# Optimization experiments

Hardware: AMD Instinct MI355X
Metric: run time of the kernel (lower is better)

The kernel has to match this reference:

```python
import jax, jax.numpy as jnp
import numpy as np

B, T, D, R = 4, 2048, 1024, 32


def setup_inputs() -> dict:
    key = jax.random.key(0)
    kx, ku = jax.random.split(key)
    x = jax.random.normal(kx, (B, T, D), dtype=jnp.float32)
    # low-rank metric factor; small init so distances are moderate
    U = jax.random.normal(ku, (D, R), dtype=jnp.float32) * 0.05
    return {"x": x, "U": U}


def reference(x, U):
    # g = U @ U.T (PSD low-rank metric).
    # dist_sq[b,t,j] = (x_t - x_j)^T g (x_t - x_j)
    #               = ||U^T x_t||^2 + ||U^T x_j||^2 - 2 (U^T x_t).(U^T x_j)
    # Algebraic expansion of the original O(B*T*T*D) broadcasted diff tensor.
    y = jnp.einsum('btd,dr->btr', x, U)                # [B,T,R]
    n = jnp.sum(y * y, axis=-1)                         # [B,T]
    cross = jnp.einsum('btr,bjr->btj', y, y)            # [B,T,T]
    dist_sq = n[:, :, None] + n[:, None, :] - 2.0 * cross
    attn = jax.nn.softmax(-dist_sq, axis=-1)            # [B,T,T]
    return jnp.einsum('btj,bjd->btd', attn, x)          # [B,T,D]
```

## Files before the change

kernel.cpp:

```cpp
#include <hip/hip_runtime.h>

#define B_ 4
#define T_ 2048
#define D_ 1024
#define R_ 32
#define XP 136

typedef __attribute__((ext_vector_type(8))) short short8;
typedef __attribute__((ext_vector_type(4))) float f32x4;
typedef __attribute__((ext_vector_type(4))) unsigned short us4;
typedef __attribute__((ext_vector_type(8))) unsigned short us8;

__device__ __forceinline__ unsigned short f2bf(float f) {
  union { float f; unsigned u; } v; v.f = f;
  unsigned r = (v.u + 0x7fffu + ((v.u >> 16) & 1u)) >> 16;
  return (unsigned short)r;
}
__device__ __forceinline__ float bf2f(unsigned short h) {
  union { unsigned u; float f; } v; v.u = (unsigned)h << 16;
  return v.f;
}

__global__ __launch_bounds__(256)
void geo_prep(const float* __restrict__ x, const float* __restrict__ U,
              unsigned short* __restrict__ xt, float* __restrict__ ypart) {
  __shared__ unsigned short xs[128 * XP];
  __shared__ unsigned short uts[32 * XP];
  const int bb = blockIdx.y, t0 = blockIdx.x * 128, d0 = blockIdx.z * 128;
  const int tid = threadIdx.x, w = tid >> 6, lane = tid & 63;
  const int m = lane & 15, quad = lane >> 4;

  f32x4 uv[4];
  #pragma unroll
  for (int p = 0; p < 4; p++) {
    const int i4 = p * 256 + tid;
    uv[p] = *(const f32x4*)(U + (size_t)(d0 + (i4 >> 3)) * R_ + (i4 & 7) * 4);
  }
  f32x4 xv[16];
  #pragma unroll
  for (int p = 0; p < 16; p++) {
    const int i4 = p * 256 + tid;
    xv[p] = *(const f32x4*)(x + ((size_t)bb * T_ + t0 + (i4 >> 5)) * D_ + d0 + (i4 & 31) * 4);
  }
  #pragma unroll
  for (int p = 0; p < 4; p++) {
    const int i4 = p * 256 + tid; const int du = i4 >> 3, ru4 = i4 & 7;
    #pragma unroll
    for (int k = 0; k < 4; k++) uts[(ru4 * 4 + k) * XP + du] = f2bf(uv[p][k]);
  }
  #pragma unroll
  for (int p = 0; p < 16; p++) {
    const int i4 = p * 256 + tid; const int r = i4 >> 5, c4 = i4 & 31;
    us4 c;
    c[0] = f2bf(xv[p][0]); c[1] = f2bf(xv[p][1]);
    c[2] = f2bf(xv[p][2]); c[3] = f2bf(xv[p][3]);
    *(us4*)&xs[r * XP + c4 * 4] = c;
  }
  __syncthreads();
  {
    const int d = tid >> 1, th = tid & 1;
    unsigned short* xo = xt + ((size_t)bb * D_ + d0 + d) * T_ + t0 + th * 64;
    #pragma unroll
    for (int i = 0; i < 8; i++) {
      us8 o;
      #pragma unroll
      for (int k = 0; k < 8; k++) o[k] = xs[(th * 64 + i * 8 + k) * XP + d];
      *(us8*)(xo + i * 8) = o;
    }
  }
  f32x4 acc[2][2];
  #pragma unroll
  for (int i = 0; i < 2; i++)
    #pragma unroll
    for (int j = 0; j < 2; j++) acc[i][j] = (f32x4){0.f, 0.f, 0.f, 0.f};
  #pragma unroll
  for (int ks = 0; ks < 4; ks++) {
    const int ko = ks * 32 + quad * 8;
    short8 a0 = *(const short8*)&xs[(w * 32 + m) * XP + ko];
    short8 a1 = *(const short8*)&xs[(w * 32 + 16 + m) * XP + ko];
    short8 b0 = *(const short8*)&uts[m * XP + ko];
    short8 b1 = *(const short8*)&uts[(16 + m) * XP + ko];
    acc[0][0] = __builtin_amdgcn_mfma_f32_16x16x32_bf16(a0, b0, acc[0][0], 0, 0, 0);
    acc[0][1] = __builtin_amdgcn_mfma_f32_16x16x32_bf16(a0, b1, acc[0][1], 0, 0, 0);
    acc[1][0] = __builtin_amdgcn_mfma_f32_16x16x32_bf16(a1, b0, acc[1][0], 0, 0, 0);
    acc[1][1] = __builtin_amdgcn_mfma_f32_16x16x32_bf16(a1, b1, acc[1][1], 0, 0, 0);
  }
  #pragma unroll
  for (int tb = 0; tb < 2; tb++)
    #pragma unroll
    for (int nb = 0; nb < 2; nb++)
      *(f32x4*)(ypart + ((size_t)(blockIdx.z * B_ + bb) * R_ + nb * 16 + m) * T_
                + t0 + w * 32 + tb * 16 + quad * 4) = acc[tb][nb];
}

__global__ __launch_bounds__(256)
void geo_reduce(const float* __restrict__ ypart, unsigned short* __restrict__ ybf,
                float* __restrict__ nsq) {
  __shared__ float ls[32][36];
  const int t0 = blockIdx.x * 32, bb = blockIdx.y;
  const int tid = threadIdx.x;
  {
    const int r = tid >> 3, t4 = (tid & 7) * 4;
    f32x4 v = {0.f, 0.f, 0.f, 0.f};
    #pragma unroll
    for (int s = 0; s < 8; s++) {
      f32x4 p = *(const f32x4*)(ypart + ((size_t)(s * B_ + bb) * R_ + r) * T_ + t0 + t4);
      #pragma unroll
      for (int k = 0; k < 4; k++) v[k] += p[k];
    }
    *(f32x4*)&ls[r][t4] = v;
  }
  __syncthreads();
  const int t = tid >> 3, r4 = (tid & 7) * 4;
  us4 pk; float part = 0.f;
  #pragma unroll
  for (int k = 0; k < 4; k++) {
    const unsigned short h = f2bf(1.69864446f * ls[r4 + k][t]);
    const float bv = bf2f(h); part += bv * bv; pk[k] = h;
  }
  *(us4*)(ybf + ((size_t)bb * T_ + t0 + t) * R_ + r4) = pk;
  part += __shfl_xor(part, 1, 64);
  part += __shfl_xor(part, 2, 64);
  part += __shfl_xor(part, 4, 64);
  if ((tid & 7) == 0) nsq[bb * T_ + t0 + t] = 0.5f * part;
}

__global__ __launch_bounds__(256, 2)
void geo_fused(const unsigned short* __restrict__ ybf,
               const float* __restrict__ nsq,
               const unsigned short* __restrict__ xt,
               float* __restrict__ out) {
  __shared__ unsigned short Bs[2][128 * 64];
  __shared__ float l_s[128];
  const int bz = blockIdx.z, id = blockIdx.x;
  const int d0 = (id & 7) * 128;
  const int t0 = (id >> 3) * 128;
  const int tid = threadIdx.x, w = tid >> 6, lane = tid & 63;
  const int m = lane & 15, quad = lane >> 4;
  const int srow = lane >> 3, sslot = lane & 7;

  const unsigned short* yb = ybf + (size_t)bz * T_ * R_;
  const float* nq = nsq + bz * T_;
  const unsigned short* Xb = xt + ((size_t)bz * D_ + d0) * T_;

#define STAGE(J0, BUF) do {                                                      \
    _Pragma("unroll")                                                            \
    for (int cc = 0; cc < 4; cc++) {                                             \
      const int rbase = w * 32 + cc * 8;                                         \
      const int row = rbase + srow;                                              \
      const int sw = (sslot ^ (row & 7)) * 8;                                    \
      __builtin_amdgcn_global_load_lds(                                          \
        (const __attribute__((address_space(1))) void*)(Xb + (size_t)row * T_ + (J0) + sw), \
        (__attribute__((address_space(3))) void*)(&Bs[BUF][rbase * 64]), 16, 0, 0); \
    } } while (0)

#define BODY(IT, AJC, NJC, AJN, NJN, BUFC, BUFN) do {                            \
    const int j0b = (IT) * 64;                                                   \
    const int jn0 = (((IT) + 1) & 31) * 64;                                      \
    _Pragma("unroll")                                                            \
    for (int ja = 0; ja < 4; ja++) {                                             \
      const int jr = 32 * (ja >> 1) + 8 * (m >> 2) + (ja & 1) * 4 + (m & 3);     \
      AJN[ja] = *(const short8*)(yb + (size_t)(jn0 + jr) * R_ + quad * 8);       \
      NJN[ja] = *(const f32x4*)(nq + jn0 + 32 * (ja >> 1) + (ja & 1) * 4 + 8 * quad); \
    }                                                                            \
    short8 pfrag[2][2];                                                          \
    _Pragma("unroll")                                                            \
    for (int tb = 0; tb < 2; tb++) {                                             \
      _Pragma("unroll")                                                          \
      for (int ja = 0; ja < 4; ja++) {                                           \
        f32x4 cin;                                                               \
        _Pragma("unroll")                                                        \
        for (int r = 0; r < 4; r++) cin[r] = nnt[tb] - NJC[ja][r];               \
        f32x4 c = __builtin_amdgcn_mfma_f32_16x16x32_bf16(AJC[ja], at[tb], cin, 0, 0, 0); \
        _Pragma("unroll")                                                        \
        for (int r = 0; r < 4; r++) {                                            \
          const float p = __builtin_amdgcn_exp2f(c[r]);                          \
          lsum4[tb][r] += p;                                                     \
          pfrag[tb][ja >> 1][(ja & 1) * 4 + r] = (short)f2bf(p);                 \
        }                                                                        \
      }                                                                          \
    }                                                                            \
    __syncthreads();                    \
    if ((IT) + 1 < 32) STAGE(j0b + 64, BUFN);                                    \
    _Pragma("unroll")                                                            \
    for (int kb = 0; kb < 2; kb++) {                                             \
      short8 bfr[8];                                                             \
      _Pragma("unroll")                                                          \
      for (int nb = 0; nb < 8; nb++)                                             \
        bfr[nb] = *(const short8*)&Bs[BUFC][(nb * 16 + m) * 64 + (((kb * 4 + quad) ^ (m & 7)) * 8)]; \
      _Pragma("unroll")                                                          \
      for (int tb = 0; tb < 2; tb++)                                             \
        _Pragma("unroll")                                                        \
        for (int nb = 0; nb < 8; nb++)                                           \
          acc[tb][nb] = __builtin_amdgcn_mfma_f32_16x16x32_bf16(pfrag[tb][kb], bfr[nb], acc[tb][nb], 0, 0, 0); \
    } } while (0)

  short8 at[2]; float nnt[2]; f32x4 lsum4[2];
  #pragma unroll
  for (int tb = 0; tb < 2; tb++) {
    at[tb] = *(const short8*)(yb + (size_t)(t0 + w * 32 + tb * 16 + m) * R_ + quad * 8);
    nnt[tb] = -nq[t0 + w * 32 + tb * 16 + m];
    lsum4[tb] = (f32x4){0.f, 0.f, 0.f, 0.f};
  }

  f32x4 acc[2][8];
  #pragma unroll
  for (int i = 0; i < 2; i++)
    #pragma unroll
    for (int j = 0; j < 8; j++) acc[i][j] = (f32x4){0.f, 0.f, 0.f, 0.f};

  short8 ajA[4], ajB[4]; f32x4 njA[4], njB[4];
  #pragma unroll
  for (int ja = 0; ja < 4; ja++) {
    const int jr = 32 * (ja >> 1) + 8 * (m >> 2) + (ja & 1) * 4 + (m & 3);
    ajA[ja] = *(const short8*)(yb + (size_t)jr * R_ + quad * 8);
    njA[ja] = *(const f32x4*)(nq + 32 * (ja >> 1) + (ja & 1) * 4 + 8 * quad);
  }
  STAGE(0, 0);

  for (int it2 = 0; it2 < 16; it2++) {
    const int it0 = it2 * 2;
    BODY(it0,     ajA, njA, ajB, njB, 0, 1);
    BODY(it0 + 1, ajB, njB, ajA, njA, 1, 0);
  }

  float lsum[2];
  #pragma unroll
  for (int tb = 0; tb < 2; tb++) {
    lsum[tb] = lsum4[tb][0] + lsum4[tb][1] + lsum4[tb][2] + lsum4[tb][3];
    lsum[tb] += __shfl_xor(lsum[tb], 16, 64);
    lsum[tb] += __shfl_xor(lsum[tb], 32, 64);
  }
  if (quad == 0) { l_s[w * 32 + m] = lsum[0]; l_s[w * 32 + 16 + m] = lsum[1]; }
  __syncthreads();
  #pragma unroll
  for (int tb = 0; tb < 2; tb++) {
    f32x4 lv = *(const f32x4*)&l_s[w * 32 + tb * 16 + quad * 4];
    f32x4 inv;
    #pragma unroll
    for (int r = 0; r < 4; r++) inv[r] = 1.f / lv[r];
    float* ob = out + ((size_t)bz * T_ + t0 + w * 32 + tb * 16 + quad * 4) * D_ + d0;
    #pragma unroll
    for (int nb = 0; nb < 8; nb++)
      #pragma unroll
      for (int r = 0; r < 4; r++)
        ob[(size_t)r * D_ + nb * 16 + m] = acc[tb][nb][r] * inv[r];
  }
#undef BODY
#undef STAGE
}

extern "C" void kernel_launch(void* const* d_in, const int* in_sizes, int n_in,
                              void* d_out, int out_size, void* d_ws, size_t ws_size,
                              hipStream_t stream) {
  const float* x = (const float*)d_in[0];
  const float* U = (const float*)d_in[1];
  float* out = (float*)d_out;

  const size_t xt_b  = (size_t)B_ * D_ * T_ * 2;
  const size_t ybf_b = (size_t)B_ * T_ * R_ * 2;
  const size_t nsq_b = (size_t)B_ * T_ * 4;
  const size_t yp_b  = (size_t)8 * B_ * R_ * T_ * 4;

  char* wp = (char*)d_ws;
  unsigned short* xtp = (unsigned short*)wp;                 wp += xt_b;
  unsigned short* ybf = (unsigned short*)wp;                 wp += ybf_b;
  float* nsq = (float*)wp;                                   wp += nsq_b;
  float* ypart = (float*)wp;                                 wp += yp_b;
  (void)ws_size; (void)in_sizes; (void)n_in; (void)out_size;

  hipLaunchKernelGGL(geo_prep, dim3(T_ / 128, B_, D_ / 128), dim3(256), 0, stream,
                     x, U, xtp, ypart);
  hipLaunchKernelGGL(geo_reduce, dim3(T_ / 32, B_), dim3(256), 0, stream,
                     ypart, ybf, nsq);
  hipLaunchKernelGGL(geo_fused, dim3((T_ / 128) * (D_ / 128), 1, B_), dim3(256), 0, stream,
                     ybf, nsq, xtp, out);
}
```

Before: 175.4 us.

## Halve fused attention row tile, raise occupancy, swizzle prep LDS transpose

The fused kernel now handles 64 query rows per block instead of 128, one 16-row tile per wave. That halves the accumulator registers and lets launch bounds ask for 4 blocks per CU. It drops the register double-buffering of key fragments in favour of a simple per-iteration load, and packs bf16 pairs with the hardware conversion. The prep kernel gets an XOR-swizzled LDS layout and a vectorized transpose to cut bank conflicts. The trade-off is that each X tile and the exp work over the key dimension are now redone for twice as many query blocks.

```diff
diff --git a/kernel.cpp b/kernel.cpp
--- a/kernel.cpp
+++ b/kernel.cpp
@@ -1,4 +1,5 @@
 #include <hip/hip_runtime.h>
+#include <hip/hip_bf16.h>
 
 #define B_ 4
 #define T_ 2048
@@ -19,6 +20,11 @@
 __device__ __forceinline__ float bf2f(unsigned short h) {
   union { unsigned u; float f; } v; v.u = (unsigned)h << 16;
   return v.f;
+}
+__device__ __forceinline__ unsigned pk2bf(float a, float b) {
+  union { __hip_bfloat162 h; unsigned u; } v;
+  v.h = __float22bfloat162_rn(make_float2(a, b));
+  return v.u;
 }
 
 __global__ __launch_bounds__(256)
@@ -51,21 +57,25 @@
   #pragma unroll
   for (int p = 0; p < 16; p++) {
     const int i4 = p * 256 + tid; const int r = i4 >> 5, c4 = i4 & 31;
-    us4 c;
-    c[0] = f2bf(xv[p][0]); c[1] = f2bf(xv[p][1]);
-    c[2] = f2bf(xv[p][2]); c[3] = f2bf(xv[p][3]);
-    *(us4*)&xs[r * XP + c4 * 4] = c;
+    union { us4 c; unsigned u[2]; } cc;
+    cc.u[0] = pk2bf(xv[p][0], xv[p][1]);
+    cc.u[1] = pk2bf(xv[p][2], xv[p][3]);
+    *(us4*)&xs[r * XP + ((c4 >> 1) ^ (r & 7)) * 8 + (c4 & 1) * 4] = cc.c;
   }
   __syncthreads();
   {
-    const int d = tid >> 1, th = tid & 1;
-    unsigned short* xo = xt + ((size_t)bb * D_ + d0 + d) * T_ + t0 + th * 64;
-    #pragma unroll
-    for (int i = 0; i < 8; i++) {
+    const int ts = tid & 15, dsb = tid >> 4;
+    us8 rowv[8];
+    #pragma unroll
+    for (int k = 0; k < 8; k++)
+      rowv[k] = *(const us8*)&xs[(ts * 8 + k) * XP + ((dsb ^ k) * 8)];
+    unsigned short* xo = xt + ((size_t)bb * D_ + d0 + dsb * 8) * T_ + t0 + ts * 8;
+    #pragma unroll
+    for (int dd = 0; dd < 8; dd++) {
       us8 o;
       #pragma unroll
-      for (int k = 0; k < 8; k++) o[k] = xs[(th * 64 + i * 8 + k) * XP + d];
-      *(us8*)(xo + i * 8) = o;
+      for (int k = 0; k < 8; k++) o[k] = rowv[k][dd];
+      *(us8*)(xo + (size_t)dd * T_) = o;
     }
   }
   f32x4 acc[2][2];
@@ -76,8 +86,9 @@
   #pragma unroll
   for (int ks = 0; ks < 4; ks++) {
     const int ko = ks * 32 + quad * 8;
-    short8 a0 = *(const short8*)&xs[(w * 32 + m) * XP + ko];
-    short8 a1 = *(const short8*)&xs[(w * 32 + 16 + m) * XP + ko];
+    const int go = ((ks * 4 + quad) ^ (m & 7)) * 8;
+    short8 a0 = *(const short8*)&xs[(w * 32 + m) * XP + go];
+    short8 a1 = *(const short8*)&xs[(w * 32 + 16 + m) * XP + go];
     short8 b0 = *(const short8*)&uts[m * XP + ko];
     short8 b1 = *(const short8*)&uts[(16 + m) * XP + ko];
     acc[0][0] = __builtin_amdgcn_mfma_f32_16x16x32_bf16(a0, b0, acc[0][0], 0, 0, 0);
@@ -125,19 +136,20 @@
   if ((tid & 7) == 0) nsq[bb * T_ + t0 + t] = 0.5f * part;
 }
 
-__global__ __launch_bounds__(256, 2)
+__global__ __launch_bounds__(256, 4)
 void geo_fused(const unsigned short* __restrict__ ybf,
                const float* __restrict__ nsq,
                const unsigned short* __restrict__ xt,
                float* __restrict__ out) {
   __shared__ unsigned short Bs[2][128 * 64];
-  __shared__ float l_s[128];
+  __shared__ float l_s[64];
   const int bz = blockIdx.z, id = blockIdx.x;
   const int d0 = (id & 7) * 128;
-  const int t0 = (id >> 3) * 128;
+  const int t0 = (id >> 3) * 64;
   const int tid = threadIdx.x, w = tid >> 6, lane = tid & 63;
   const int m = lane & 15, quad = lane >> 4;
   const int srow = lane >> 3, sslot = lane & 7;
+  const int tw = w * 16;
 
   const unsigned short* yb = ybf + (size_t)bz * T_ * R_;
   const float* nq = nsq + bz * T_;
@@ -154,99 +166,71 @@
         (__attribute__((address_space(3))) void*)(&Bs[BUF][rbase * 64]), 16, 0, 0); \
     } } while (0)
 
-#define BODY(IT, AJC, NJC, AJN, NJN, BUFC, BUFN) do {                            \
-    const int j0b = (IT) * 64;                                                   \
-    const int jn0 = (((IT) + 1) & 31) * 64;                                      \
-    _Pragma("unroll")                                                            \
-    for (int ja = 0; ja < 4; ja++) {                                             \
-      const int jr = 32 * (ja >> 1) + 8 * (m >> 2) + (ja & 1) * 4 + (m & 3);     \
-      AJN[ja] = *(const short8*)(yb + (size_t)(jn0 + jr) * R_ + quad * 8);       \
-      NJN[ja] = *(const f32x4*)(nq + jn0 + 32 * (ja >> 1) + (ja & 1) * 4 + 8 * quad); \
-    }                                                                            \
-    short8 pfrag[2][2];                                                          \
-    _Pragma("unroll")                                                            \
-    for (int tb = 0; tb < 2; tb++) {                                             \
-      _Pragma("unroll")                                                          \
-      for (int ja = 0; ja < 4; ja++) {                                           \
-        f32x4 cin;                                                               \
-        _Pragma("unroll")                                                        \
-        for (int r = 0; r < 4; r++) cin[r] = nnt[tb] - NJC[ja][r];               \
-        f32x4 c = __builtin_amdgcn_mfma_f32_16x16x32_bf16(AJC[ja], at[tb], cin, 0, 0, 0); \
-        _Pragma("unroll")                                                        \
-        for (int r = 0; r < 4; r++) {                                            \
-          const float p = __builtin_amdgcn_exp2f(c[r]);                          \
-          lsum4[tb][r] += p;                                                     \
-          pfrag[tb][ja >> 1][(ja & 1) * 4 + r] = (short)f2bf(p);                 \
-        }                                                                        \
-      }                                                                          \
-    }                                                                            \
-    __syncthreads();                    \
-    if ((IT) + 1 < 32) STAGE(j0b + 64, BUFN);                                    \
-    _Pragma("unroll")                                                            \
-    for (int kb = 0; kb < 2; kb++) {                                             \
-      short8 bfr[8];                                                             \
-      _Pragma("unroll")                                                          \
-      for (int nb = 0; nb < 8; nb++)                                             \
-        bfr[nb] = *(const short8*)&Bs[BUFC][(nb * 16 + m) * 64 + (((kb * 4 + quad) ^ (m & 7)) * 8)]; \
-      _Pragma("unroll")                                                          \
-      for (int tb = 0; tb < 2; tb++)                                             \
-        _Pragma("unroll")                                                        \
-        for (int nb = 0; nb < 8; nb++)                                           \
-          acc[tb][nb] = __builtin_amdgcn_mfma_f32_16x16x32_bf16(pfrag[tb][kb], bfr[nb], acc[tb][nb], 0, 0, 0); \
-    } } while (0)
-
-  short8 at[2]; float nnt[2]; f32x4 lsum4[2];
-  #pragma unroll
-  for (int tb = 0; tb < 2; tb++) {
-    at[tb] = *(const short8*)(yb + (size_t)(t0 + w * 32 + tb * 16 + m) * R_ + quad * 8);
-    nnt[tb] = -nq[t0 + w * 32 + tb * 16 + m];
-    lsum4[tb] = (f32x4){0.f, 0.f, 0.f, 0.f};
-  }
-
-  f32x4 acc[2][8];
-  #pragma unroll
-  for (int i = 0; i < 2; i++)
-    #pragma unroll
-    for (int j = 0; j < 8; j++) acc[i][j] = (f32x4){0.f, 0.f, 0.f, 0.f};
-
-  short8 ajA[4], ajB[4]; f32x4 njA[4], njB[4];
-  #pragma unroll
-  for (int ja = 0; ja < 4; ja++) {
-    const int jr = 32 * (ja >> 1) + 8 * (m >> 2) + (ja & 1) * 4 + (m & 3);
-    ajA[ja] = *(const short8*)(yb + (size_t)jr * R_ + quad * 8);
-    njA[ja] = *(const f32x4*)(nq + 32 * (ja >> 1) + (ja & 1) * 4 + 8 * quad);
-  }
+  short8 at = *(const short8*)(yb + (size_t)(t0 + tw + m) * R_ + quad * 8);
+  const float nnt = -nq[t0 + tw + m];
+  f32x4 lsum4 = {0.f, 0.f, 0.f, 0.f};
+
+  f32x4 acc[8];
+  #pragma unroll
+  for (int j = 0; j < 8; j++) acc[j] = (f32x4){0.f, 0.f, 0.f, 0.f};
+
   STAGE(0, 0);
 
-  for (int it2 = 0; it2 < 16; it2++) {
-    const int it0 = it2 * 2;
-    BODY(it0,     ajA, njA, ajB, njB, 0, 1);
-    BODY(it0 + 1, ajB, njB, ajA, njA, 1, 0);
-  }
-
-  float lsum[2];
-  #pragma unroll
-  for (int tb = 0; tb < 2; tb++) {
-    lsum[tb] = lsum4[tb][0] + lsum4[tb][1] + lsum4[tb][2] + lsum4[tb][3];
-    lsum[tb] += __shfl_xor(lsum[tb], 16, 64);
-    lsum[tb] += __shfl_xor(lsum[tb], 32, 64);
-  }
-  if (quad == 0) { l_s[w * 32 + m] = lsum[0]; l_s[w * 32 + 16 + m] = lsum[1]; }
+  for (int it = 0; it < 32; ++it) {
+    const int j0 = it * 64, buf = it & 1;
+    short8 aj[4]; f32x4 njv[4];
+    #pragma unroll
+    for (int ja = 0; ja < 4; ja++) {
+      const int jr = 32 * (ja >> 1) + 8 * (m >> 2) + (ja & 1) * 4 + (m & 3);
+      aj[ja] = *(const short8*)(yb + (size_t)(j0 + jr) * R_ + quad * 8);
+      njv[ja] = *(const f32x4*)(nq + j0 + 32 * (ja >> 1) + (ja & 1) * 4 + 8 * quad);
+    }
+    union { short8 s; unsigned u[4]; } pf[2];
+    #pragma unroll
+    for (int ja = 0; ja < 4; ja++) {
+      f32x4 cin;
+      #pragma unroll
+      for (int r = 0; r < 4; r++) cin[r] = nnt - njv[ja][r];
+      f32x4 c = __builtin_amdgcn_mfma_f32_16x16x32_bf16(aj[ja], at, cin, 0, 0, 0);
+      f32x4 p;
+      #pragma unroll
+      for (int r = 0; r < 4; r++) {
+        p[r] = __builtin_amdgcn_exp2f(c[r]);
+        lsum4[r] += p[r];
+      }
+      pf[ja >> 1].u[(ja & 1) * 2 + 0] = pk2bf(p[0], p[1]);
+      pf[ja >> 1].u[(ja & 1) * 2 + 1] = pk2bf(p[2], p[3]);
+    }
+    __syncthreads();
+    if (it + 1 < 32) STAGE(j0 + 64, buf ^ 1);
+    #pragma unroll
+    for (int kb = 0; kb < 2; kb++) {
+      short8 bfr[8];
+      #pragma unroll
+      for (int nb = 0; nb < 8; nb++)
+        bfr[nb] = *(const short8*)&Bs[buf][(nb * 16 + m) * 64 + (((kb * 4 + quad) ^ (m & 7)) * 8)];
+      #pragma unroll
+      for (int nb = 0; nb < 8; nb++)
+        acc[nb] = __builtin_amdgcn_mfma_f32_16x16x32_bf16(pf[kb].s, bfr[nb], acc[nb], 0, 0, 0);
+    }
+  }
+  float lsum = lsum4[0] + lsum4[1] + lsum4[2] + lsum4[3];
+  lsum += __shfl_xor(lsum, 16, 64);
+  lsum += __shfl_xor(lsum, 32, 64);
+  if (quad == 0) l_s[tw + m] = lsum;
   __syncthreads();
-  #pragma unroll
-  for (int tb = 0; tb < 2; tb++) {
-    f32x4 lv = *(const f32x4*)&l_s[w * 32 + tb * 16 + quad * 4];
+  {
+    f32x4 lv = *(const f32x4*)&l_s[tw + quad * 4];
     f32x4 inv;
     #pragma unroll
     for (int r = 0; r < 4; r++) inv[r] = 1.f / lv[r];
-    float* ob = out + ((size_t)bz * T_ + t0 + w * 32 + tb * 16 + quad * 4) * D_ + d0;
+    float* ob = out + ((size_t)bz * T_ + t0 + tw + quad * 4) * D_ + d0;
     #pragma unroll
     for (int nb = 0; nb < 8; nb++)
       #pragma unroll
       for (int r = 0; r < 4; r++)
-        ob[(size_t)r * D_ + nb * 16 + m] = acc[tb][nb][r] * inv[r];
-  }
-#undef BODY
+        ob[(size_t)r * D_ + nb * 16 + m] = acc[nb][r] * inv[r];
+  }
 #undef STAGE
 }
 
@@ -273,6 +257,6 @@
                      x, U, xtp, ypart);
   hipLaunchKernelGGL(geo_reduce, dim3(T_ / 32, B_), dim3(256), 0, stream,
                      ypart, ybf, nsq);
-  hipLaunchKernelGGL(geo_fused, dim3((T_ / 128) * (D_ / 128), 1, B_), dim3(256), 0, stream,
+  hipLaunchKernelGGL(geo_fused, dim3((T_ / 64) * (D_ / 128), 1, B_), dim3(256), 0, stream,
                      ybf, nsq, xtp, out);
 }
```

Measured after the change: 158.7 us. 1.11x faster.
